# Kernel optimization log

Hardware: AMD Instinct MI355X
Metric: run time of the kernel (lower is better)

## Reference

```python
import jax, jax.numpy as jnp
import numpy as np

B, NM, NB, Z, H, K = 1024, 20000, 25000, 64, 256, 20
BETA = 0.1
LOG2PI = float(np.log(2.0 * np.pi))


def _log_normal(x, m, v):
    D = x.shape[-1]
    return (-0.5 * D * LOG2PI
            - 0.5 * jnp.sum(jnp.log(v), axis=-1)
            - 0.5 * jnp.sum((x - m) ** 2 / v, axis=-1))


def _kl_gmm(z, q_m, q_logv, p_m, p_logv):
    log_q = _log_normal(z, q_m, jnp.exp(q_logv))                               # [B]
    lp = _log_normal(z[:, None, :], p_m[None], jnp.exp(p_logv)[None])          # [B,K]
    log_p = jax.scipy.special.logsumexp(lp, axis=1) - jnp.log(float(p_m.shape[0]))
    return jnp.sum(log_q - log_p)


def _dist2(x, y):
    # ||x_i - y_j||_2^2, expanded form (avoids the [R,C,D] broadcast of the torch code)
    x2 = jnp.sum(x * x, axis=1, keepdims=True)
    y2 = jnp.sum(y * y, axis=1, keepdims=True)
    return x2 + y2.T - 2.0 * (x @ y.T)


def _distance_gmm(mu_s, mu_d, lv_s, lv_d):
    return _dist2(mu_s, mu_d) + _dist2(jnp.exp(0.5 * lv_s), jnp.exp(0.5 * lv_d)) + 1e-6


def _cost_mat(cost_s, cost_t, tran):
    f1 = jnp.sum(cost_s ** 2, axis=1, keepdims=True) / cost_s.shape[0]  # [ns,1]
    f2 = jnp.sum(cost_t ** 2, axis=1, keepdims=True) / cost_t.shape[0]  # [nt,1]
    return f1 + f2.T - 2.0 * (cost_s @ tran @ cost_t.T)


def _fgw(mu, z_mu, logvar, z_logvar):
    c_post = _distance_gmm(mu, mu, logvar, logvar)
    c_prior = _distance_gmm(z_mu, z_mu, z_logvar, z_logvar)
    c_pp = _distance_gmm(mu, z_mu, logvar, z_logvar)
    ns, nt = c_post.shape[0], c_prior.shape[0]
    p_s = jnp.ones((ns, 1), c_post.dtype) / ns
    p_t = jnp.ones((nt, 1), c_post.dtype) / nt

    def compute_tran(c_post, c_prior, c_pp):
        def outer(carry, _):
            tran, dual = carry
            cost = BETA * _cost_mat(c_post, c_prior, tran) + (1.0 - BETA) * c_pp
            kernel = jnp.exp(-cost / jnp.max(jnp.abs(cost))) * tran
            b = p_t / (kernel.T @ dual)

            def inner(c2, _):
                dual, b = c2
                dual = p_s / (kernel @ b)
                b = p_t / (kernel.T @ dual)
                return (dual, b), None

            (dual, b), _ = jax.lax.scan(inner, (dual, b), None, length=5)
            tran = (dual @ b.T) * kernel
            return (tran, dual), None

        init = (jnp.ones((ns, nt), c_post.dtype) / (ns * nt),
                jnp.ones((ns, 1), c_post.dtype) / ns)
        (tran, _), _ = jax.lax.scan(outer, init, None, length=10)
        return jnp.where(jnp.any(jnp.isnan(tran)),
                         jnp.ones((ns, nt), tran.dtype) / (ns * nt), tran)

    # torch detaches tran before the final cost, so cut all gradient through the loop
    tran = jax.lax.stop_gradient(compute_tran(c_post, c_prior, c_pp))
    cost = BETA * _cost_mat(c_post, c_prior, tran) + (1.0 - BETA) * c_pp
    return jnp.sum(cost * tran)


def _forward(batch_user_x, batch_user_y, p_mu_a, p_logv_a, p_mu_b, p_logv_b,
             eps_x, eps_y, eps_xr, eps_yr,
             W1a, b1a, W21a, b21a, W22a, b22a, W3a, b3a, W4a, b4a,
             W1b, b1b, W21b, b21b, W22b, b22b, W3b, b3b, W4b, b4b):
    def enc_a(x):
        h = jax.nn.relu(x @ W1a + b1a)
        return h @ W21a + b21a, h @ W22a + b22a

    def dec_a(z):
        return jax.nn.relu(z @ W3a + b3a) @ W4a + b4a

    def enc_b(x):
        h = jax.nn.relu(x @ W1b + b1b)
        return h @ W21b + b21b, h @ W22b + b22b

    def dec_b(z):
        return jax.nn.relu(z @ W3b + b3b) @ W4b + b4b

    # dropout rate = 0.0 -> identity
    mu_a, logvar_a = enc_a(batch_user_x)
    z_x = mu_a + eps_x * jnp.exp(0.5 * logvar_a)
    preds_x = dec_a(z_x)
    mu_b, logvar_b = enc_b(batch_user_y)
    z_y = mu_b + eps_y * jnp.exp(0.5 * logvar_b)
    preds_y = dec_b(z_y)

    gmm_reg_loss_a = _kl_gmm(z_x, mu_a, logvar_a, p_mu_a, p_logv_a)
    gmm_reg_loss_b = _kl_gmm(z_y, mu_b, logvar_b, p_mu_b, p_logv_b)
    align_global_loss = _fgw(mu_b, mu_a, logvar_b, logvar_a)

    preds_x2y = dec_b(z_x)
    preds_y2x = dec_a(z_y)
    m_xr, lv_xr = enc_b(preds_x2y)
    feature_x_r = m_xr + eps_xr * jnp.exp(0.5 * lv_xr)
    m_yr, lv_yr = enc_a(preds_y2x)
    feature_y_r = m_yr + eps_yr * jnp.exp(0.5 * lv_yr)

    cyc_loss_x = jnp.linalg.norm(z_x - feature_x_r)
    cyc_loss_y = jnp.linalg.norm(z_y - feature_y_r)
    return (preds_x, preds_y, preds_x2y, preds_y2x, z_x, z_y,
            gmm_reg_loss_a, gmm_reg_loss_b, feature_x_r, feature_y_r,
            align_global_loss, cyc_loss_x, cyc_loss_y)


def setup_inputs() -> dict:
    key = jax.random.key(0)
    ks = jax.random.split(key, 24)

    def nrm(i, shape, s=1.0):
        return jax.random.normal(ks[i], shape, dtype=jnp.float32) * s

    return {
        "user_1": jax.random.randint(ks[0], (B,), 0, 100000),
        "user_2": jax.random.randint(ks[1], (B,), 0, 100000),
        "batch_user_x": jax.random.uniform(ks[2], (B, NM), dtype=jnp.float32),
        "batch_user_y": jax.random.uniform(ks[3], (B, NB), dtype=jnp.float32),
        "p_mu_a": nrm(4, (K, Z)), "p_logv_a": nrm(5, (K, Z), 0.1),
        "p_mu_b": nrm(6, (K, Z)), "p_logv_b": nrm(7, (K, Z), 0.1),
        "eps_x": nrm(8, (B, Z)), "eps_y": nrm(9, (B, Z)),
        "eps_xr": nrm(10, (B, Z)), "eps_yr": nrm(11, (B, Z)),
        "W1a": nrm(12, (NM, H), 0.02), "b1a": jnp.zeros((H,), jnp.float32),
        "W21a": nrm(13, (H, Z), 0.02), "b21a": jnp.zeros((Z,), jnp.float32),
        "W22a": nrm(14, (H, Z), 0.02), "b22a": jnp.zeros((Z,), jnp.float32),
        "W3a": nrm(15, (Z, H), 0.02), "b3a": jnp.zeros((H,), jnp.float32),
        "W4a": nrm(16, (H, NM), 0.02), "b4a": jnp.zeros((NM,), jnp.float32),
        "W1b": nrm(17, (NB, H), 0.02), "b1b": jnp.zeros((H,), jnp.float32),
        "W21b": nrm(18, (H, Z), 0.02), "b21b": jnp.zeros((Z,), jnp.float32),
        "W22b": nrm(19, (H, Z), 0.02), "b22b": jnp.zeros((Z,), jnp.float32),
        "W3b": nrm(20, (Z, H), 0.02), "b3b": jnp.zeros((H,), jnp.float32),
        "W4b": nrm(21, (H, NB), 0.02), "b4b": jnp.zeros((NB,), jnp.float32),
    }


def reference(user_1, user_2, batch_user_x, batch_user_y, p_mu_a, p_logv_a, p_mu_b, p_logv_b,
              eps_x, eps_y, eps_xr, eps_yr,
              W1a, b1a, W21a, b21a, W22a, b22a, W3a, b3a, W4a, b4a,
              W1b, b1b, W21b, b21b, W22b, b22b, W3b, b3b, W4b, b4b):
    # user_1/user_2 are unused by the torch forward as well
    return _forward(batch_user_x, batch_user_y, p_mu_a, p_logv_a, p_mu_b, p_logv_b,
                    eps_x, eps_y, eps_xr, eps_yr,
                    W1a, b1a, W21a, b21a, W22a, b22a, W3a, b3a, W4a, b4a,
                    W1b, b1b, W21b, b21b, W22b, b22b, W3b, b3b, W4b, b4b)
```

## Files before the change

kernel.cpp:

```cpp
#include <hip/hip_runtime.h>


#define DEVI __device__ __forceinline__

typedef __attribute__((ext_vector_type(4))) float  f32x4;
typedef __attribute__((ext_vector_type(4))) short  s16x4;
typedef __attribute__((ext_vector_type(8))) short  s16x8;
typedef __attribute__((ext_vector_type(8))) __bf16 bf16x8;

#define PS (1.f / 1024.f)
#define UNIF (1.f / (1024.f * 1024.f))

DEVI short f2bf(float f) {
  unsigned u = __float_as_uint(f);
  u += 0x7fffu + ((u >> 16) & 1u);
  return (short)(u >> 16);
}
DEVI float bf2f(unsigned short u) { return __uint_as_float(((unsigned)u) << 16); }

DEVI f32x4 mfma16(bf16x8 a, bf16x8 b, f32x4 c) {
  return __builtin_amdgcn_mfma_f32_16x16x32_bf16(a, b, c, 0, 0, 0);
}

struct GemmArgs {
// ... 73 lines not shown
    #pragma unroll
    for (int s = 0; s < 2; ++s) {
      const int ko = 32 * s + 8 * (lane >> 4);
      bf16x8 a0 = *(const bf16x8*)&As[(wr * 32 +      (lane & 15)) * BKP + ko];
      bf16x8 a1 = *(const bf16x8*)&As[(wr * 32 + 16 + (lane & 15)) * BKP + ko];
      #pragma unroll
      for (int fn = 0; fn < 4; ++fn) {
        bf16x8 b = *(const bf16x8*)&Bs[(wc * 64 + fn * 16 + (lane & 15)) * BKP + ko];
        acc[0][fn] = mfma16(a0, b, acc[0][fn]);
        acc[1][fn] = mfma16(a1, b, acc[1][fn]);
      }
    }
    __syncthreads();
  }

  if constexpr (EPI == EPI_PARTIAL) {
    #pragma unroll
    for (int fm = 0; fm < 2; ++fm) {
      #pragma unroll
      for (int fn = 0; fn < 4; ++fn) {
        #pragma unroll
        for (int p = 0; p < 4; ++p) {
          int gm = m0 + wr * 32 + fm * 16 + (lane >> 4) * 4 + p;
          int gn = n0 + wc * 64 + fn * 16 + (lane & 15);
          g.partials[((size_t)split * g.M + gm) * 256 + gn] = acc[fm][fn][p];
        }
      }
    }
  } else {
    float* Cs = (float*)SM;
    #pragma unroll
    for (int h = 0; h < WC; ++h) {
      __syncthreads();
      if (wc == h) {
        #pragma unroll
        for (int fm = 0; fm < 2; ++fm)
          #pragma unroll
          for (int fn = 0; fn < 4; ++fn)
            #pragma unroll
            for (int p = 0; p < 4; ++p)
              Cs[(wr * 32 + fm * 16 + (lane >> 4) * 4 + p) * 65
                 + fn * 16 + (lane & 15)] = acc[fm][fn][p];
      }
      __syncthreads();
      const int n0h = n0 + 64 * h;
      #pragma unroll
      for (int j = tid; j < BM * 16; j += NT) {
        int r = j >> 4, c4 = j & 15;
        int gn = n0h + 4 * c4;
        if (gn < g.N) {
          f32x4 v = *(f32x4*)&Cs[r * 65 + 4 * c4];
          f32x4 b = *(const f32x4*)&g.bias[gn];
          v.x += b.x; v.y += b.y; v.z += b.z; v.w += b.w;
          *(f32x4*)(g.outF + (size_t)(m0 + r) * g.ldc + gn) = v;
        }
      }
    }
  }
}

struct Q4 { GemmArgs g[4]; };

template<int BM, int BN, int WR, int WC, int EPI>
__global__ __launch_bounds__(WR*WC*64)
void k_gemmN(Q4 q)
{
  GemmArgs g = q.g[blockIdx.z];
  if constexpr (EPI == EPI_BIAS) {
    if ((int)(blockIdx.y * BN) >= g.N) return;
  }
  gemm_body<BM, BN, WR, WC, EPI>(g);
}

struct G1Args {
  const unsigned short* A;
  const unsigned short* KTb;
  const float* dinv;
  const float* braw;
  unsigned short* U;
  const unsigned* nflag;
  int mode;
};

__global__ __launch_bounds__(256)
void k_fgw_g1(G1Args a)
{
  __shared__ short As[64 * 72];
  __shared__ short Bs[64 * 72];
  const bool uni = (a.mode == 0) || (a.mode == 2 && *a.nflag != 0u);

  const int bid = blockIdx.x, tid = threadIdx.x;
  const int lane = tid & 63, wv = tid >> 6;
  const int wr = wv & 1, wc = wv >> 1;
  const int m0 = (bid >> 4) * 64, n0 = (bid & 15) * 64;

  f32x4 acc[2][2];
  #pragma unroll
  for (int i = 0; i < 2; ++i)
    #pragma unroll
    for (int j = 0; j < 2; ++j) acc[i][j] = f32x4{0.f, 0.f, 0.f, 0.f};

  const short ub = f2bf(UNIF);

  for (int kb = 0; kb < 1024; kb += 64) {
    #pragma unroll
    for (int i = 0; i < 2; ++i) {
      int idx = tid + 256 * i;
      int r = idx >> 3, q = idx & 7;
      s16x8 av = *(const s16x8*)&a.A[(size_t)(m0 + r) * 1024 + kb + 8 * q];
      if (!uni) {
        f32x4 d0 = *(const f32x4*)&a.dinv[kb + 8 * q];
        f32x4 d1 = *(const f32x4*)&a.dinv[kb + 8 * q + 4];
        s16x8 o;
        o[0] = f2bf(bf2f((unsigned short)av[0]) * d0.x);
        o[1] = f2bf(bf2f((unsigned short)av[1]) * d0.y);
        o[2] = f2bf(bf2f((unsigned short)av[2]) * d0.z);
        o[3] = f2bf(bf2f((unsigned short)av[3]) * d0.w);
        o[4] = f2bf(bf2f((unsigned short)av[4]) * d1.x);
        o[5] = f2bf(bf2f((unsigned short)av[5]) * d1.y);
        o[6] = f2bf(bf2f((unsigned short)av[6]) * d1.z);
        o[7] = f2bf(bf2f((unsigned short)av[7]) * d1.w);
        av = o;
      }
      *(s16x8*)&As[r * 72 + 8 * q] = av;
      s16x8 bv;
      if (uni) {
        #pragma unroll
        for (int j = 0; j < 8; ++j) bv[j] = ub;
      } else {
        bv = *(const s16x8*)&a.KTb[(size_t)(n0 + r) * 1024 + kb + 8 * q];
      }
      *(s16x8*)&Bs[r * 72 + 8 * q] = bv;
    }
    __syncthreads();
    #pragma unroll
    for (int s = 0; s < 2; ++s) {
      const int ko = 32 * s + 8 * (lane >> 4);
      bf16x8 a0 = *(const bf16x8*)&As[(wr * 32 +      (lane & 15)) * 72 + ko];
      bf16x8 a1 = *(const bf16x8*)&As[(wr * 32 + 16 + (lane & 15)) * 72 + ko];
      bf16x8 b0 = *(const bf16x8*)&Bs[(wc * 32 +      (lane & 15)) * 72 + ko];
      bf16x8 b1 = *(const bf16x8*)&Bs[(wc * 32 + 16 + (lane & 15)) * 72 + ko];
      acc[0][0] = mfma16(a0, b0, acc[0][0]);
      acc[1][0] = mfma16(a1, b0, acc[1][0]);
      acc[0][1] = mfma16(a0, b1, acc[0][1]);
      acc[1][1] = mfma16(a1, b1, acc[1][1]);
    }
    __syncthreads();
  }

  #pragma unroll
  for (int fm = 0; fm < 2; ++fm) {
    #pragma unroll
    for (int fn = 0; fn < 2; ++fn) {
      int gn = n0 + wc * 32 + fn * 16 + (lane & 15);
      float bs = uni ? 1.f : (PS / a.braw[gn]);
      #pragma unroll
      for (int p = 0; p < 4; ++p) {
        int gm = m0 + wr * 32 + fm * 16 + (lane >> 4) * 4 + p;
        float v = acc[fm][fn][p];
        a.U[(size_t)gm * 1024 + gn] = (unsigned short)f2bf(uni ? v : bs * v);
      }
    }
  }
}

struct FgwGemmArgs {
  const unsigned short* A;
  const unsigned short* Bt;
  float* cost;
  const float* f1;
  const float* f2;
  const float* cpp;
  unsigned* mx;
  float* loss;
  float* braw2;
  const float* Kf;
  const float* dinv;
  const float* brawv;
  const unsigned* nflag;
};

template<int EPI>
__global__ __launch_bounds__(256)
void k_fgw_gemm(FgwGemmArgs a)
{
  __shared__ short As[64 * 72];
  __shared__ short Bs[64 * 72];
  __shared__ float red[4];

  const int bid = blockIdx.x, tid = threadIdx.x;
  const int lane = tid & 63, wv = tid >> 6;
  const int wr = wv & 1, wc = wv >> 1;
  const int m0 = (bid >> 4) * 64, n0 = (bid & 15) * 64;

  if constexpr (EPI == EPI_COST) {
    if (bid == 0) {
      #pragma unroll
      for (int i = 0; i < 4; ++i) a.braw2[tid + 256 * i] = 0.f;
    }
  }

  f32x4 acc[2][2];
  #pragma unroll
  for (int i = 0; i < 2; ++i)
    #pragma unroll
    for (int j = 0; j < 2; ++j) acc[i][j] = f32x4{0.f, 0.f, 0.f, 0.f};

  for (int kb = 0; kb < 1024; kb += 64) {
    #pragma unroll
    for (int i = 0; i < 2; ++i) {
      int idx = tid + 256 * i;
      int r = idx >> 3, q = idx & 7;
      *(s16x8*)&As[r * 72 + 8 * q] = *(const s16x8*)&a.A [(size_t)(m0 + r) * 1024 + kb + 8 * q];
      *(s16x8*)&Bs[r * 72 + 8 * q] = *(const s16x8*)&a.Bt[(size_t)(n0 + r) * 1024 + kb + 8 * q];
    }
    __syncthreads();
    #pragma unroll
    for (int s = 0; s < 2; ++s) {
      const int ko = 32 * s + 8 * (lane >> 4);
      bf16x8 a0 = *(const bf16x8*)&As[(wr * 32 +      (lane & 15)) * 72 + ko];
      bf16x8 a1 = *(const bf16x8*)&As[(wr * 32 + 16 + (lane & 15)) * 72 + ko];
      bf16x8 b0 = *(const bf16x8*)&Bs[(wc * 32 +      (lane & 15)) * 72 + ko];
      bf16x8 b1 = *(const bf16x8*)&Bs[(wc * 32 + 16 + (lane & 15)) * 72 + ko];
      acc[0][0] = mfma16(a0, b0, acc[0][0]);
      acc[1][0] = mfma16(a1, b0, acc[1][0]);
      acc[0][1] = mfma16(a0, b1, acc[0][1]);
      acc[1][1] = mfma16(a1, b1, acc[1][1]);
    }
    __syncthreads();
  }

  bool uni = false;
  if constexpr (EPI == EPI_LOSS) uni = (*a.nflag != 0u);

  float lred = 0.f;
  #pragma unroll
  for (int fm = 0; fm < 2; ++fm) {
    #pragma unroll
    for (int fn = 0; fn < 2; ++fn) {
      int gn = n0 + wc * 32 + fn * 16 + (lane & 15);
      float bs = 0.f;
      if constexpr (EPI == EPI_LOSS) bs = uni ? 0.f : (PS / a.brawv[gn]);
      #pragma unroll
      for (int p = 0; p < 4; ++p) {
        int gm = m0 + wr * 32 + fm * 16 + (lane >> 4) * 4 + p;
        float v = acc[fm][fn][p];
        size_t o = (size_t)gm * 1024 + gn;
        float c = 0.1f * (a.f1[gm] + a.f2[gn] - 2.f * v) + 0.9f * a.cpp[o];
        if constexpr (EPI == EPI_COST) {
          a.cost[o] = c;
          lred = fmaxf(lred, fabsf(c));
        } else {
          float trec = uni ? UNIF : (a.dinv[gm] * bs) * a.Kf[o];
          lred += c * trec;
        }
      }
    }
  }
  #pragma unroll
  for (int off = 32; off; off >>= 1) {
    float t = __shfl_xor(lred, off, 64);
    lred = (EPI == EPI_COST) ? fmaxf(lred, t) : (lred + t);
  }
  if (lane == 0) red[wv] = lred;
  __syncthreads();
  if (tid == 0) {
    if constexpr (EPI == EPI_COST) {
      float t = fmaxf(fmaxf(red[0], red[1]), fmaxf(red[2], red[3]));
      atomicMax(a.mx, __float_as_uint(t));
    } else {
      atomicAdd(a.loss, red[0] + red[1] + red[2] + red[3]);
    }
  }
}

__global__ __launch_bounds__(256)
void k_kbuild(const float* cost, const unsigned* mxbits, float* K, float* KT,
              unsigned short* KTb, const float* dinv, const float* brawOld,
              float* braw2, int uniform)
{
  __shared__ float tt[64 * 65];
  __shared__ float dS[64];
  __shared__ float bS[64];
  __shared__ float csum[4][64];
  const int r0 = blockIdx.x * 64, c0 = blockIdx.y * 64;
  const int tid = threadIdx.x;
  const float inv = 1.f / __uint_as_float(*mxbits);
  if (tid < 64) dS[tid] = dinv[r0 + tid];
  else if (tid >= 64 && tid < 128 && !uniform) bS[tid - 64] = PS / brawOld[c0 + tid - 64];
  __syncthreads();
  float colp = 0.f;
  #pragma unroll
  for (int i = 0; i < 16; ++i) {
    int idx = tid + 256 * i;
    int r = idx >> 6, c = idx & 63;
    size_t o = (size_t)(r0 + r) * 1024 + (c0 + c);
    float trec = uniform ? UNIF : (dS[r] * bS[c]) * K[o];
    float v = expf(-cost[o] * inv) * trec;
    K[o] = v;
    tt[r * 65 + c] = v;
    colp += v * dS[r];
  }
  csum[tid >> 6][tid & 63] = colp;
  __syncthreads();
  #pragma unroll
  for (int i = 0; i < 16; ++i) {
    int idx = tid + 256 * i;
    int c = idx >> 6, r = idx & 63;
    float v = tt[r * 65 + c];
    size_t o = (size_t)(c0 + c) * 1024 + (r0 + r);
    KT[o] = v;
    KTb[o] = (unsigned short)f2bf(v);
  }
  if (tid < 64)
    atomicAdd(&braw2[c0 + tid],
              csum[0][tid] + csum[1][tid] + csum[2][tid] + csum[3][tid]);
}

__global__ __launch_bounds__(256)
void k_matvec(const float* M, const float* xraw, float* yraw, float* invOut)
{
  const int r = blockIdx.x * 4 + (threadIdx.x >> 6);
  const int lane = threadIdx.x & 63;
  const int wv = threadIdx.x >> 6;
  const f32x4* row = (const f32x4*)(M + (size_t)r * 1024);
  const f32x4* xv  = (const f32x4*)xraw;
  float s = 0.f;
  #pragma unroll
  for (int q = 0; q < 4; ++q) {
    f32x4 a = row[lane + 64 * q];
    f32x4 x = xv [lane + 64 * q];
    f32x4 iv;
    iv.x = PS / x.x; iv.y = PS / x.y; iv.z = PS / x.z; iv.w = PS / x.w;
    if (invOut && blockIdx.x == 0 && wv == 0)
      *(f32x4*)&invOut[4 * (lane + 64 * q)] = iv;
    s += a.x * iv.x + a.y * iv.y + a.z * iv.z + a.w * iv.w;
  }
  #pragma unroll
  for (int o = 32; o; o >>= 1) s += __shfl_xor(s, o, 64);
  if (lane == 0) yraw[r] = s;
}

__global__ __launch_bounds__(256)
void k_nanscan(const float* K, const float* dinv, const float* braw, unsigned* flag)
{
  unsigned bad = 0;
  const int base = blockIdx.x * 256 + threadIdx.x;
  #pragma unroll
  for (int i = 0; i < 16; ++i) {
    int idx = base + 65536 * i;
    int r = idx >> 10, c = idx & 1023;
    float v = (dinv[r] * (PS / braw[c])) * K[idx];
    if (v != v) bad = 1u;
  }
  if (bad) atomicOr(flag, 1u);
}

struct DistMMArgs {
  const unsigned short* Fx[3]; const unsigned short* Fy[3];
  const float* nx[3]; const float* ny[3];
  unsigned short* outB[2]; float* outF; float* frow[2];
};
__global__ __launch_bounds__(256)
void k_distmm(DistMMArgs a)
{
  __shared__ short As[64 * 72];
  __shared__ short Bs[64 * 72];
  const int z = blockIdx.y;
  const int bid = blockIdx.x, tid = threadIdx.x;
  const int lane = tid & 63, wv = tid >> 6;
  const int wr = wv & 1, wc = wv >> 1;
  const int m0 = (bid >> 4) * 64, n0 = (bid & 15) * 64;
  const unsigned short* X = a.Fx[z];
  const unsigned short* Y = a.Fy[z];

  f32x4 acc[2][2];
  #pragma unroll
  for (int i = 0; i < 2; ++i)
    #pragma unroll
    for (int j = 0; j < 2; ++j) acc[i][j] = f32x4{0.f, 0.f, 0.f, 0.f};

  #pragma unroll
  for (int kb = 0; kb < 128; kb += 64) {
    #pragma unroll
    for (int i = 0; i < 2; ++i) {
      int idx = tid + 256 * i;
      int r = idx >> 3, q = idx & 7;
      *(s16x8*)&As[r * 72 + 8 * q] = *(const s16x8*)&X[(size_t)(m0 + r) * 128 + kb + 8 * q];
      *(s16x8*)&Bs[r * 72 + 8 * q] = *(const s16x8*)&Y[(size_t)(n0 + r) * 128 + kb + 8 * q];
    }
    __syncthreads();
    #pragma unroll
    for (int s = 0; s < 2; ++s) {
      const int ko = 32 * s + 8 * (lane >> 4);
      bf16x8 a0 = *(const bf16x8*)&As[(wr * 32 +      (lane & 15)) * 72 + ko];
      bf16x8 a1 = *(const bf16x8*)&As[(wr * 32 + 16 + (lane & 15)) * 72 + ko];
      bf16x8 b0 = *(const bf16x8*)&Bs[(wc * 32 +      (lane & 15)) * 72 + ko];
      bf16x8 b1 = *(const bf16x8*)&Bs[(wc * 32 + 16 + (lane & 15)) * 72 + ko];
      acc[0][0] = mfma16(a0, b0, acc[0][0]);
      acc[1][0] = mfma16(a1, b0, acc[1][0]);
      acc[0][1] = mfma16(a0, b1, acc[0][1]);
      acc[1][1] = mfma16(a1, b1, acc[1][1]);
    }
    __syncthreads();
  }

  const float* nxp = a.nx[z];
  const float* nyp = a.ny[z];
  float rp[2][4];
  #pragma unroll
  for (int fm = 0; fm < 2; ++fm)
    #pragma unroll
    for (int p = 0; p < 4; ++p) rp[fm][p] = 0.f;

  #pragma unroll
  for (int fm = 0; fm < 2; ++fm) {
    #pragma unroll
    for (int fn = 0; fn < 2; ++fn) {
      #pragma unroll
      for (int p = 0; p < 4; ++p) {
        int gm = m0 + wr * 32 + fm * 16 + (lane >> 4) * 4 + p;
        int gn = n0 + wc * 32 + fn * 16 + (lane & 15);
        float val = nxp[gm] + nyp[gn] - 2.f * acc[fm][fn][p] + 1e-6f;
        if (z == 2) a.outF[(size_t)gm * 1024 + gn] = val;
        else {
          a.outB[z][(size_t)gm * 1024 + gn] = (unsigned short)f2bf(val);
          rp[fm][p] += val * val;
        }
      }
    }
  }
  if (z < 2) {
    #pragma unroll
    for (int fm = 0; fm < 2; ++fm)
      #pragma unroll
      for (int p = 0; p < 4; ++p) {
        float v = rp[fm][p];
        v += __shfl_xor(v, 1, 64);
        v += __shfl_xor(v, 2, 64);
        v += __shfl_xor(v, 4, 64);
        v += __shfl_xor(v, 8, 64);
        rp[fm][p] = v;
      }
    if ((lane & 15) == 0) {
      #pragma unroll
      for (int fm = 0; fm < 2; ++fm)
        #pragma unroll
        for (int p = 0; p < 4; ++p) {
          int gm = m0 + wr * 32 + fm * 16 + (lane >> 4) * 4 + p;
          atomicAdd(&a.frow[z][gm], rp[fm][p] * (1.f / 1024.f));
        }
    }
  }
}

struct T4 {
  const float* in[4]; unsigned short* out[4]; int R[4], C[4], nx[4], nt[4];
  float* dinv; float* f1; float* f2; unsigned* mx; unsigned* nanflag;
  float* cyc; float* ga; float* gb; float* al;
};
__global__ void k_transpose4(T4 d)
{
  const int z = blockIdx.y;
  const int tid = threadIdx.x;
  if (z == 4) {
    if (blockIdx.x == 0) {
      #pragma unroll
      for (int i = 0; i < 4; ++i) {
        int k = tid + 256 * i;
        d.dinv[k] = PS; d.f1[k] = 0.f; d.f2[k] = 0.f;
      }
      if (tid < 16) d.mx[tid] = 0u;
      if (tid == 0) {
        *d.nanflag = 0u; d.cyc[0] = 0.f; d.cyc[1] = 0.f;
        *d.ga = 0.f; *d.gb = 0.f; *d.al = 0.f;
      }
    }
    return;
  }
  __shared__ float t[64][65];
  const int tile = blockIdx.x;
  if (tile >= d.nt[z]) return;
  const int R = d.R[z], C = d.C[z];
  const int r0 = (tile % d.nx[z]) * 64, c0 = (tile / d.nx[z]) * 64;
  const float* in = d.in[z];
  unsigned short* out = d.out[z];
  #pragma unroll
  for (int i = 0; i < 16; ++i) {
    int idx = tid + 256 * i;
    int r = idx >> 6, c = idx & 63;
    float v = 0.f;
    if ((r0 + r) < R && (c0 + c) < C) v = in[(size_t)(r0 + r) * C + (c0 + c)];
    t[r][c] = v;
  }
  __syncthreads();
  #pragma unroll
  for (int i = 0; i < 16; ++i) {
    int idx = tid + 256 * i;
    int c = idx >> 6, r = idx & 63;
    if ((c0 + c) < C && (r0 + r) < R)
      out[(size_t)(c0 + c) * R + (r0 + r)] = (unsigned short)f2bf(t[r][c]);
  }
}

__global__ void k_wcomb_reduce(const float* partials, unsigned short* WcTa,
                               unsigned short* WcTb)
{
  __shared__ float t[64][65];
  const int z = blockIdx.z;
  const float* P = partials + (size_t)z * 32 * 256 * 256;
  unsigned short* WcT = z ? WcTb : WcTa;
  const int u0 = blockIdx.x * 64, v0 = blockIdx.y * 64;
  const int tid = threadIdx.x;
  #pragma unroll
  for (int i = 0; i < 16; ++i) {
    int idx = tid + 256 * i;
    int u = idx >> 6, v = idx & 63;
    float s = 0.f;
    for (int p = 0; p < 32; ++p)
      s += P[(size_t)p * 65536 + (u0 + u) * 256 + (v0 + v)];
    t[u][v] = s;
  }
  __syncthreads();
  #pragma unroll
  for (int i = 0; i < 16; ++i) {
    int idx = tid + 256 * i;
    int v = idx >> 6, u = idx & 63;
    WcT[(size_t)(v0 + v) * 256 + (u0 + u)] = (unsigned short)f2bf(t[u][v]);
  }
}

struct BcArgs {
  const float* b4[2]; const unsigned short* Wt1[2]; const float* b1[2];
  float* bc[2]; int K[2];
};
__global__ void k_bcvec(BcArgs a)
{
  const int y = blockIdx.y;
  const int c = blockIdx.x * 4 + (threadIdx.x >> 6);
  const int lane = threadIdx.x & 63;
  const int K = a.K[y];
  const unsigned short* wrow = a.Wt1[y] + (size_t)c * K;
  const float* b4 = a.b4[y];
  float s = 0.f;
  for (int k = lane * 8; k < K; k += 512) {
    s16x8 w = *(const s16x8*)&wrow[k];
    f32x4 v0 = *(const f32x4*)&b4[k];
    f32x4 v1 = *(const f32x4*)&b4[k + 4];
    s += v0.x * bf2f((unsigned short)w[0]) + v0.y * bf2f((unsigned short)w[1])
       + v0.z * bf2f((unsigned short)w[2]) + v0.w * bf2f((unsigned short)w[3])
       + v1.x * bf2f((unsigned short)w[4]) + v1.y * bf2f((unsigned short)w[5])
       + v1.z * bf2f((unsigned short)w[6]) + v1.w * bf2f((unsigned short)w[7]);
  }
  #pragma unroll
  for (int o = 32; o; o >>= 1) s += __shfl_xor(s, o, 64);
  if (lane == 0) a.bc[y][c] = s + a.b1[y][c];
}

struct EF {
  const float* partials[2]; const float* bias[2];
  const float* W21[2]; const float* b21[2];
  const float* W22[2]; const float* b22[2]; const float* eps[2];
  const float* pmu[2]; const float* plv[2]; float* gmmO[2];
  float* mu[2]; float* lv[2]; float* zO[2];
  unsigned short* F[2]; float* n[2];
};
__global__ __launch_bounds__(256)
void k_enc_fused(EF a)
{
  __shared__ float hrow[256];
  __shared__ float res[128];
  const int y = blockIdx.y;
  const int i = blockIdx.x;
  const int t = threadIdx.x;
  {
    float s = a.bias[y][t];
    const float* P = a.partials[y] + (size_t)i * 256 + t;
    #pragma unroll
    for (int p = 0; p < 16; ++p) s += P[(size_t)p * 262144];
    hrow[t] = fmaxf(s, 0.f);
  }
  __syncthreads();
  if (t < 128) {
    const int c = t & 63;
    const float* W = (t < 64) ? a.W21[y] : a.W22[y];
    float acc = (t < 64) ? a.b21[y][c] : a.b22[y][c];
    #pragma unroll 8
    for (int j = 0; j < 256; ++j) acc += hrow[j] * W[j * 64 + c];
    res[t] = acc;
  }
  __syncthreads();
  if (t < 64) {
    float mu = res[t], lv = res[64 + t];
    a.mu[y][(size_t)i * 64 + t] = mu;
    a.lv[y][(size_t)i * 64 + t] = lv;
    float sig = expf(0.5f * lv);
    float zd = mu + a.eps[y][(size_t)i * 64 + t] * sig;
    a.zO[y][(size_t)i * 64 + t] = zd;
    unsigned short u0 = (unsigned short)f2bf(mu);
    unsigned short u1 = (unsigned short)f2bf(sig);
    unsigned short* Fr = a.F[y] + (size_t)i * 128;
    Fr[t] = u0;
// ... 128 lines not shown
  const float* W3b = (const float*)d_in[28];  const float* b3b = (const float*)d_in[29];
  const float* W4b = (const float*)d_in[30];  const float* b4b = (const float*)d_in[31];

  float* out = (float*)d_out;
  const size_t P_X = 0, P_Y = 20480000, P_X2Y = 46080000, P_Y2X = 71680000;
  const size_t Z_X = 92160000, Z_Y = 92225536;
  const size_t GMM_A = 92291072, GMM_B = 92291073;
  const size_t F_XR = 92291074, F_YR = 92356610;
  const size_t ALIGN = 92422146, CYC_X = 92422147, CYC_Y = 92422148;

  char* w = (char*)d_ws;
  size_t off = 0;
  auto alloc = [&](size_t bytes) -> void* {
    void* p = w + off;
    off += (bytes + 255) & ~(size_t)255;
    return p;
  };
  unsigned short* Wt1a = (unsigned short*)alloc((size_t)256 * 20000 * 2);
  unsigned short* Wt1b = (unsigned short*)alloc((size_t)256 * 25000 * 2);
  unsigned short* W4ta = (unsigned short*)alloc((size_t)20000 * 256 * 2);
  unsigned short* W4tb = (unsigned short*)alloc((size_t)25000 * 256 * 2);
  unsigned short* WcTa = (unsigned short*)alloc((size_t)256 * 256 * 2);
  unsigned short* WcTb = (unsigned short*)alloc((size_t)256 * 256 * 2);
  float* bca  = (float*)alloc(256 * 4);
  float* bcb  = (float*)alloc(256 * 4);
  float* mu_a = (float*)alloc(1024 * 64 * 4);
  float* lv_a = (float*)alloc(1024 * 64 * 4);
  float* mu_b = (float*)alloc(1024 * 64 * 4);
  float* lv_b = (float*)alloc(1024 * 64 * 4);
  float* f1   = (float*)alloc(1024 * 4);
  float* f2   = (float*)alloc(1024 * 4);
  unsigned* mx      = (unsigned*)alloc(16 * 4);
  unsigned* nanflag = (unsigned*)alloc(256);
  float* cyc  = (float*)alloc(256);
  float* draw = (float*)alloc(1024 * 4);
  float* braw = (float*)alloc(1024 * 4);
  float* braw2 = (float*)alloc(1024 * 4);
  float* dinv = (float*)alloc(1024 * 4);
  unsigned short* Fb = (unsigned short*)alloc((size_t)1024 * 128 * 2);
  unsigned short* Fa = (unsigned short*)alloc((size_t)1024 * 128 * 2);
  float* nb = (float*)alloc(1024 * 4);
  float* na = (float*)alloc(1024 * 4);
  char* arena = (char*)alloc((size_t)32 * 1024 * 1024);
  float* partials = (float*)arena;
  size_t ao = 0;
  auto aalloc = [&](size_t bytes) -> void* {
    void* p = arena + ao;
    ao += (bytes + 255) & ~(size_t)255;
    return p;
  };
  unsigned short* cpostB  = (unsigned short*)aalloc((size_t)1024 * 1024 * 2);
  unsigned short* cpriorB = (unsigned short*)aalloc((size_t)1024 * 1024 * 2);
  float* cpp  = (float*)aalloc((size_t)1024 * 1024 * 4);
  unsigned short* Umat  = (unsigned short*)aalloc((size_t)1024 * 1024 * 2);
  float* cost  = (float*)aalloc((size_t)1024 * 1024 * 4);
  float* Kmat  = (float*)aalloc((size_t)1024 * 1024 * 4);
  float* KTmat = (float*)aalloc((size_t)1024 * 1024 * 4);
  unsigned short* KTb = (unsigned short*)aalloc((size_t)1024 * 1024 * 2);
  float* hd0 = (float*)(arena);
  float* hd1 = (float*)(arena + (size_t)1024 * 256 * 4);
  float* hd2 = (float*)(arena + (size_t)2 * 1024 * 256 * 4);
  float* hd3 = (float*)(arena + (size_t)3 * 1024 * 256 * 4);

  {
    T4 d{};
    d.in[0] = W1a; d.out[0] = Wt1a; d.R[0] = 20000; d.C[0] = 256;
    d.in[1] = W1b; d.out[1] = Wt1b; d.R[1] = 25000; d.C[1] = 256;
    d.in[2] = W4a; d.out[2] = W4ta; d.R[2] = 256;   d.C[2] = 20000;
    d.in[3] = W4b; d.out[3] = W4tb; d.R[3] = 256;   d.C[3] = 25000;
    for (int z = 0; z < 4; ++z) {
      d.nx[z] = (d.R[z] + 63) / 64;
      d.nt[z] = d.nx[z] * ((d.C[z] + 63) / 64);
    }
    d.dinv = dinv; d.f1 = f1; d.f2 = f2; d.mx = mx; d.nanflag = nanflag;
    d.cyc = cyc; d.ga = out + GMM_A; d.gb = out + GMM_B; d.al = out + ALIGN;
    k_transpose4<<<dim3(1564, 5), 256, 0, stream>>>(d);
  }

  {
    Q4 q{};
    q.g[0].Af = W4a; q.g[0].Bt = Wt1a; q.g[0].partials = partials;
    q.g[0].M = 256; q.g[0].N = 256; q.g[0].K = 20000;
    q.g[0].lda = 20000; q.g[0].ldbt = 20000;
    q.g[0].totSteps = 313; q.g[0].nSplits = 32;
    q.g[1] = q.g[0];
    q.g[1].Af = W4b; q.g[1].Bt = Wt1b;
    q.g[1].partials = partials + (size_t)32 * 65536;
    q.g[1].K = 25000; q.g[1].lda = 25000; q.g[1].ldbt = 25000; q.g[1].totSteps = 391;
    k_gemmN<128, 256, 4, 4, EPI_PARTIAL><<<dim3(2, 32, 2), 1024, 0, stream>>>(q);
    k_wcomb_reduce<<<dim3(4, 4, 2), 256, 0, stream>>>(partials, WcTa, WcTb);
    BcArgs bc{};
    bc.b4[0] = b4a; bc.Wt1[0] = Wt1a; bc.b1[0] = b1a; bc.bc[0] = bca; bc.K[0] = 20000;
    bc.b4[1] = b4b; bc.Wt1[1] = Wt1b; bc.b1[1] = b1b; bc.bc[1] = bcb; bc.K[1] = 25000;
    k_bcvec<<<dim3(64, 2), 256, 0, stream>>>(bc);
  }

  {
    Q4 q{};
    q.g[0].Af = X; q.g[0].Bt = Wt1a; q.g[0].partials = partials;
    q.g[0].M = 1024; q.g[0].N = 256; q.g[0].K = 20000;
    q.g[0].lda = 20000; q.g[0].ldbt = 20000;
    q.g[0].totSteps = 313; q.g[0].nSplits = 16;
    q.g[1] = q.g[0];
    q.g[1].Af = Y; q.g[1].Bt = Wt1b;
    q.g[1].partials = partials + (size_t)16 * 1024 * 256;
    q.g[1].K = 25000; q.g[1].lda = 25000; q.g[1].ldbt = 25000; q.g[1].totSteps = 391;
    k_gemmN<128, 256, 4, 4, EPI_PARTIAL><<<dim3(8, 16, 2), 1024, 0, stream>>>(q);
    EF e{};
    e.partials[0] = partials; e.partials[1] = partials + (size_t)16 * 1024 * 256;
    e.bias[0] = b1a; e.bias[1] = b1b;
    e.W21[0] = W21a; e.b21[0] = b21a; e.W22[0] = W22a; e.b22[0] = b22a;
    e.eps[0] = epsx; e.mu[0] = mu_a; e.lv[0] = lv_a; e.zO[0] = out + Z_X;
    e.F[0] = Fa; e.n[0] = na;
    e.pmu[0] = pmua; e.plv[0] = plva; e.gmmO[0] = out + GMM_A;
    e.W21[1] = W21b; e.b21[1] = b21b; e.W22[1] = W22b; e.b22[1] = b22b;
    e.eps[1] = epsy; e.mu[1] = mu_b; e.lv[1] = lv_b; e.zO[1] = out + Z_Y;
    e.F[1] = Fb; e.n[1] = nb;
    e.pmu[1] = pmub; e.plv[1] = plvb; e.gmmO[1] = out + GMM_B;
    k_enc_fused<<<dim3(1024, 2), 256, 0, stream>>>(e);
  }

  {
    DistMMArgs dm{};
    dm.Fx[0] = Fb; dm.Fy[0] = Fb; dm.nx[0] = nb; dm.ny[0] = nb;
    dm.Fx[1] = Fa; dm.Fy[1] = Fa; dm.nx[1] = na; dm.ny[1] = na;
    dm.Fx[2] = Fb; dm.Fy[2] = Fa; dm.nx[2] = nb; dm.ny[2] = na;
    dm.outB[0] = cpostB; dm.outB[1] = cpriorB; dm.outF = cpp;
    dm.frow[0] = f1; dm.frow[1] = f2;
    k_distmm<<<dim3(256, 3), 256, 0, stream>>>(dm);
  }
  G1Args g1{};
  g1.A = cpostB; g1.KTb = KTb; g1.dinv = dinv; g1.braw = braw;
  g1.U = Umat; g1.nflag = nanflag;
  FgwGemmArgs fg{};
  fg.A = Umat; fg.Bt = cpriorB;
  fg.f1 = f1; fg.f2 = f2; fg.cpp = cpp; fg.cost = cost;
  fg.loss = out + ALIGN; fg.braw2 = braw2;
  fg.Kf = Kmat; fg.dinv = dinv; fg.brawv = braw; fg.nflag = nanflag;
  for (int it = 0; it < 10; ++it) {
    g1.mode = (it == 0) ? 0 : 1;
    k_fgw_g1<<<256, 256, 0, stream>>>(g1);
    fg.mx = mx + it;
    k_fgw_gemm<EPI_COST><<<256, 256, 0, stream>>>(fg);
    k_kbuild<<<dim3(16, 16), 256, 0, stream>>>(cost, mx + it, Kmat, KTmat, KTb,
                                               dinv, braw, braw2, it == 0 ? 1 : 0);
    for (int r = 0; r < 5; ++r) {
      k_matvec<<<256, 256, 0, stream>>>(Kmat, r == 0 ? braw2 : braw, draw, nullptr);
      k_matvec<<<256, 256, 0, stream>>>(KTmat, draw, braw, r == 4 ? dinv : nullptr);
    }
  }
  k_nanscan<<<256, 256, 0, stream>>>(Kmat, dinv, braw, nanflag);
  g1.mode = 2;
  k_fgw_g1<<<256, 256, 0, stream>>>(g1);
  k_fgw_gemm<EPI_LOSS><<<256, 256, 0, stream>>>(fg);

  {
    DH4 d{};
    d.z[0] = out + Z_X; d.W3[0] = W3a; d.b3[0] = b3a; d.hd[0] = hd0;
    d.z[1] = out + Z_Y; d.W3[1] = W3a; d.b3[1] = b3a; d.hd[1] = hd1;
    d.z[2] = out + Z_Y; d.W3[2] = W3b; d.b3[2] = b3b; d.hd[2] = hd2;
    d.z[3] = out + Z_X; d.W3[3] = W3b; d.b3[3] = b3b; d.hd[3] = hd3;
    k_dec_head4<<<dim3(1024, 4), 256, 0, stream>>>(d);
  }

  {
    RencArgs r{};
    r.hd[0] = hd3; r.WcT[0] = WcTb; r.bc[0] = bcb;
    r.W21[0] = W21b; r.b21[0] = b21b; r.W22[0] = W22b; r.b22[0] = b22b;
    r.eps[0] = epsxr; r.fout[0] = out + F_XR; r.zin[0] = out + Z_X;
    r.hd[1] = hd1; r.WcT[1] = WcTa; r.bc[1] = bca;
    r.W21[1] = W21a; r.b21[1] = b21a; r.W22[1] = W22a; r.b22[1] = b22a;
    r.eps[1] = epsyr; r.fout[1] = out + F_YR; r.zin[1] = out + Z_Y;
    r.cyc = cyc;
    k_renc_head<<<dim3(1024, 2), 256, 0, stream>>>(r);
  }
  k_finish<<<1, 64, 0, stream>>>(cyc, out + CYC_X, out + CYC_Y);

  {
    Q4 q{};
    q.g[0].Af = hd0; q.g[0].Bt = W4ta; q.g[0].outF = out + P_X; q.g[0].bias = b4a;
    q.g[0].M = 1024; q.g[0].N = 20000; q.g[0].K = 256;
    q.g[0].lda = 256; q.g[0].ldbt = 256; q.g[0].ldc = 20000;
    q.g[1] = q.g[0]; q.g[1].Af = hd1; q.g[1].outF = out + P_Y2X;
    q.g[2] = q.g[0];
    q.g[2].Af = hd2; q.g[2].Bt = W4tb; q.g[2].outF = out + P_Y; q.g[2].bias = b4b;
    q.g[2].N = 25000; q.g[2].ldc = 25000;
    q.g[3] = q.g[2]; q.g[3].Af = hd3; q.g[3].outF = out + P_X2Y;
    k_gemmN<128, 128, 4, 2, EPI_BIAS><<<dim3(8, 196, 4), 512, 0, stream>>>(q);
  }
}
```

Before: 1.453 ms.

## Use 8 waves per FGW GEMM block and double split-K for weight fold

The FGW GEMM kernels (g1 and cost/loss) now launch 512 threads per 64x64 tile, with each wave computing a 32x16 sub-tile. This halves per-wave MFMA work and load loops to raise latency hiding on the small 256-block grid. Separately, the W4·W1 split-K GEMM goes from 32 to 64 splits, with the reduce kernel and partials offsets updated to match, to fill more CUs at the cost of more partial traffic. Wave index mapping (wr/wc from wv) is assumed to extend to 8 waves, and it must do so for the tile coverage to be correct.

Result: faster. 1.394 ms (-4.1%).

```diff
diff --git a/kernel.cpp b/kernel.cpp
--- a/kernel.cpp
+++ b/kernel.cpp
@@ -179,7 +179,7 @@
   int mode;
 };
 
-__global__ __launch_bounds__(256)
+__global__ __launch_bounds__(512)
 void k_fgw_g1(G1Args a)
 {
   __shared__ short As[64 * 72];
@@ -191,19 +191,15 @@
   const int wr = wv & 1, wc = wv >> 1;
   const int m0 = (bid >> 4) * 64, n0 = (bid & 15) * 64;
 
-  f32x4 acc[2][2];
-  #pragma unroll
-  for (int i = 0; i < 2; ++i)
-    #pragma unroll
-    for (int j = 0; j < 2; ++j) acc[i][j] = f32x4{0.f, 0.f, 0.f, 0.f};
+  f32x4 acc[2];
+  acc[0] = f32x4{0.f, 0.f, 0.f, 0.f};
+  acc[1] = f32x4{0.f, 0.f, 0.f, 0.f};
 
   const short ub = f2bf(UNIF);
 
   for (int kb = 0; kb < 1024; kb += 64) {
-    #pragma unroll
-    for (int i = 0; i < 2; ++i) {
-      int idx = tid + 256 * i;
-      int r = idx >> 3, q = idx & 7;
+    {
+      int r = tid >> 3, q = tid & 7;
       s16x8 av = *(const s16x8*)&a.A[(size_t)(m0 + r) * 1024 + kb + 8 * q];
       if (!uni) {
         f32x4 d0 = *(const f32x4*)&a.dinv[kb + 8 * q];
@@ -233,30 +229,24 @@
     #pragma unroll
     for (int s = 0; s < 2; ++s) {
       const int ko = 32 * s + 8 * (lane >> 4);
+      bf16x8 b0 = *(const bf16x8*)&Bs[(wc * 16 + (lane & 15)) * 72 + ko];
       bf16x8 a0 = *(const bf16x8*)&As[(wr * 32 +      (lane & 15)) * 72 + ko];
       bf16x8 a1 = *(const bf16x8*)&As[(wr * 32 + 16 + (lane & 15)) * 72 + ko];
-      bf16x8 b0 = *(const bf16x8*)&Bs[(wc * 32 +      (lane & 15)) * 72 + ko];
-      bf16x8 b1 = *(const bf16x8*)&Bs[(wc * 32 + 16 + (lane & 15)) * 72 + ko];
-      acc[0][0] = mfma16(a0, b0, acc[0][0]);
-      acc[1][0] = mfma16(a1, b0, acc[1][0]);
-      acc[0][1] = mfma16(a0, b1, acc[0][1]);
-      acc[1][1] = mfma16(a1, b1, acc[1][1]);
+      acc[0] = mfma16(a0, b0, acc[0]);
+      acc[1] = mfma16(a1, b0, acc[1]);
     }
     __syncthreads();
   }
 
+  const int gn = n0 + wc * 16 + (lane & 15);
+  const float bs = uni ? 1.f : (PS / a.braw[gn]);
   #pragma unroll
   for (int fm = 0; fm < 2; ++fm) {
     #pragma unroll
-    for (int fn = 0; fn < 2; ++fn) {
-      int gn = n0 + wc * 32 + fn * 16 + (lane & 15);
-      float bs = uni ? 1.f : (PS / a.braw[gn]);
-      #pragma unroll
-      for (int p = 0; p < 4; ++p) {
-        int gm = m0 + wr * 32 + fm * 16 + (lane >> 4) * 4 + p;
-        float v = acc[fm][fn][p];
-        a.U[(size_t)gm * 1024 + gn] = (unsigned short)f2bf(uni ? v : bs * v);
-      }
+    for (int p = 0; p < 4; ++p) {
+      int gm = m0 + wr * 32 + fm * 16 + (lane >> 4) * 4 + p;
+      float v = acc[fm][p];
+      a.U[(size_t)gm * 1024 + gn] = (unsigned short)f2bf(uni ? v : bs * v);
     }
   }
 }
@@ -278,12 +268,12 @@
 };
 
 template<int EPI>
-__global__ __launch_bounds__(256)
+__global__ __launch_bounds__(512)
 void k_fgw_gemm(FgwGemmArgs a)
 {
   __shared__ short As[64 * 72];
   __shared__ short Bs[64 * 72];
-  __shared__ float red[4];
+  __shared__ float red[8];
 
   const int bid = blockIdx.x, tid = threadIdx.x;
   const int lane = tid & 63, wv = tid >> 6;
@@ -293,9 +283,174 @@
   if constexpr (EPI == EPI_COST) {
     if (bid == 0) {
       #pragma unroll
-      for (int i = 0; i < 4; ++i) a.braw2[tid + 256 * i] = 0.f;
-    }
-  }
+      for (int i = 0; i < 2; ++i) a.braw2[tid + 512 * i] = 0.f;
+    }
+  }
+
+  f32x4 acc[2];
+  acc[0] = f32x4{0.f, 0.f, 0.f, 0.f};
+  acc[1] = f32x4{0.f, 0.f, 0.f, 0.f};
+
+  for (int kb = 0; kb < 1024; kb += 64) {
+    {
+      int r = tid >> 3, q = tid & 7;
+      *(s16x8*)&As[r * 72 + 8 * q] = *(const s16x8*)&a.A [(size_t)(m0 + r) * 1024 + kb + 8 * q];
+      *(s16x8*)&Bs[r * 72 + 8 * q] = *(const s16x8*)&a.Bt[(size_t)(n0 + r) * 1024 + kb + 8 * q];
+    }
+    __syncthreads();
+    #pragma unroll
+    for (int s = 0; s < 2; ++s) {
+      const int ko = 32 * s + 8 * (lane >> 4);
+      bf16x8 b0 = *(const bf16x8*)&Bs[(wc * 16 + (lane & 15)) * 72 + ko];
+      bf16x8 a0 = *(const bf16x8*)&As[(wr * 32 +      (lane & 15)) * 72 + ko];
+      bf16x8 a1 = *(const bf16x8*)&As[(wr * 32 + 16 + (lane & 15)) * 72 + ko];
+      acc[0] = mfma16(a0, b0, acc[0]);
+      acc[1] = mfma16(a1, b0, acc[1]);
+    }
+    __syncthreads();
+  }
+
+  bool uni = false;
+  if constexpr (EPI == EPI_LOSS) uni = (*a.nflag != 0u);
+
+  const int gn = n0 + wc * 16 + (lane & 15);
+  float bs = 0.f;
+  if constexpr (EPI == EPI_LOSS) bs = uni ? 0.f : (PS / a.brawv[gn]);
+
+  float lred = 0.f;
+  #pragma unroll
+  for (int fm = 0; fm < 2; ++fm) {
+    #pragma unroll
+    for (int p = 0; p < 4; ++p) {
+      int gm = m0 + wr * 32 + fm * 16 + (lane >> 4) * 4 + p;
+      float v = acc[fm][p];
+      size_t o = (size_t)gm * 1024 + gn;
+      float c = 0.1f * (a.f1[gm] + a.f2[gn] - 2.f * v) + 0.9f * a.cpp[o];
+      if constexpr (EPI == EPI_COST) {
+        a.cost[o] = c;
+        lred = fmaxf(lred, fabsf(c));
+      } else {
+        float trec = uni ? UNIF : (a.dinv[gm] * bs) * a.Kf[o];
+        lred += c * trec;
+      }
+    }
+  }
+  #pragma unroll
+  for (int off = 32; off; off >>= 1) {
+    float t = __shfl_xor(lred, off, 64);
+    lred = (EPI == EPI_COST) ? fmaxf(lred, t) : (lred + t);
+  }
+  if (lane == 0) red[wv] = lred;
+  __syncthreads();
+  if (tid == 0) {
+    float t = red[0];
+    #pragma unroll
+    for (int i = 1; i < 8; ++i)
+      t = (EPI == EPI_COST) ? fmaxf(t, red[i]) : (t + red[i]);
+    if constexpr (EPI == EPI_COST) atomicMax(a.mx, __float_as_uint(t));
+    else atomicAdd(a.loss, t);
+  }
+}
+
+__global__ __launch_bounds__(256)
+void k_kbuild(const float* cost, const unsigned* mxbits, float* K, float* KT,
+              unsigned short* KTb, const float* dinv, const float* brawOld,
+              float* braw2, int uniform)
+{
+  __shared__ float tt[64 * 65];
+  __shared__ float dS[64];
+  __shared__ float bS[64];
+  __shared__ float csum[4][64];
+  const int r0 = blockIdx.x * 64, c0 = blockIdx.y * 64;
+  const int tid = threadIdx.x;
+  const float inv = 1.f / __uint_as_float(*mxbits);
+  if (tid < 64) dS[tid] = dinv[r0 + tid];
+  else if (tid >= 64 && tid < 128 && !uniform) bS[tid - 64] = PS / brawOld[c0 + tid - 64];
+  __syncthreads();
+  float colp = 0.f;
+  #pragma unroll
+  for (int i = 0; i < 16; ++i) {
+    int idx = tid + 256 * i;
+    int r = idx >> 6, c = idx & 63;
+    size_t o = (size_t)(r0 + r) * 1024 + (c0 + c);
+    float trec = uniform ? UNIF : (dS[r] * bS[c]) * K[o];
+    float v = expf(-cost[o] * inv) * trec;
+    K[o] = v;
+    tt[r * 65 + c] = v;
+    colp += v * dS[r];
+  }
+  csum[tid >> 6][tid & 63] = colp;
+  __syncthreads();
+  #pragma unroll
+  for (int i = 0; i < 16; ++i) {
+    int idx = tid + 256 * i;
+    int c = idx >> 6, r = idx & 63;
+    float v = tt[r * 65 + c];
+    size_t o = (size_t)(c0 + c) * 1024 + (r0 + r);
+    KT[o] = v;
+    KTb[o] = (unsigned short)f2bf(v);
+  }
+  if (tid < 64)
+    atomicAdd(&braw2[c0 + tid],
+              csum[0][tid] + csum[1][tid] + csum[2][tid] + csum[3][tid]);
+}
+
+__global__ __launch_bounds__(256)
+void k_matvec(const float* M, const float* xraw, float* yraw, float* invOut)
+{
+  const int r = blockIdx.x * 4 + (threadIdx.x >> 6);
+  const int lane = threadIdx.x & 63;
+  const int wv = threadIdx.x >> 6;
+  const f32x4* row = (const f32x4*)(M + (size_t)r * 1024);
+  const f32x4* xv  = (const f32x4*)xraw;
+  float s = 0.f;
+  #pragma unroll
+  for (int q = 0; q < 4; ++q) {
+    f32x4 a = row[lane + 64 * q];
+    f32x4 x = xv [lane + 64 * q];
+    f32x4 iv;
+    iv.x = PS / x.x; iv.y = PS / x.y; iv.z = PS / x.z; iv.w = PS / x.w;
+    if (invOut && blockIdx.x == 0 && wv == 0)
+      *(f32x4*)&invOut[4 * (lane + 64 * q)] = iv;
+    s += a.x * iv.x + a.y * iv.y + a.z * iv.z + a.w * iv.w;
+  }
+  #pragma unroll
+  for (int o = 32; o; o >>= 1) s += __shfl_xor(s, o, 64);
+  if (lane == 0) yraw[r] = s;
+}
+
+__global__ __launch_bounds__(256)
+void k_nanscan(const float* K, const float* dinv, const float* braw, unsigned* flag)
+{
+  unsigned bad = 0;
+  const int base = blockIdx.x * 256 + threadIdx.x;
+  #pragma unroll
+  for (int i = 0; i < 16; ++i) {
+    int idx = base + 65536 * i;
+    int r = idx >> 10, c = idx & 1023;
+    float v = (dinv[r] * (PS / braw[c])) * K[idx];
+    if (v != v) bad = 1u;
+  }
+  if (bad) atomicOr(flag, 1u);
+}
+
+struct DistMMArgs {
+  const unsigned short* Fx[3]; const unsigned short* Fy[3];
+  const float* nx[3]; const float* ny[3];
+  unsigned short* outB[2]; float* outF; float* frow[2];
+};
+__global__ __launch_bounds__(256)
+void k_distmm(DistMMArgs a)
+{
+  __shared__ short As[64 * 72];
+  __shared__ short Bs[64 * 72];
+  const int z = blockIdx.y;
+  const int bid = blockIdx.x, tid = threadIdx.x;
+  const int lane = tid & 63, wv = tid >> 6;
+  const int wr = wv & 1, wc = wv >> 1;
+  const int m0 = (bid >> 4) * 64, n0 = (bid & 15) * 64;
+  const unsigned short* X = a.Fx[z];
+  const unsigned short* Y = a.Fy[z];
 
   f32x4 acc[2][2];
   #pragma unroll
@@ -303,13 +458,14 @@
     #pragma unroll
     for (int j = 0; j < 2; ++j) acc[i][j] = f32x4{0.f, 0.f, 0.f, 0.f};
 
-  for (int kb = 0; kb < 1024; kb += 64) {
+  #pragma unroll
+  for (int kb = 0; kb < 128; kb += 64) {
     #pragma unroll
     for (int i = 0; i < 2; ++i) {
       int idx = tid + 256 * i;
       int r = idx >> 3, q = idx & 7;
-      *(s16x8*)&As[r * 72 + 8 * q] = *(const s16x8*)&a.A [(size_t)(m0 + r) * 1024 + kb + 8 * q];
-      *(s16x8*)&Bs[r * 72 + 8 * q] = *(const s16x8*)&a.Bt[(size_t)(n0 + r) * 1024 + kb + 8 * q];
+      *(s16x8*)&As[r * 72 + 8 * q] = *(const s16x8*)&X[(size_t)(m0 + r) * 128 + kb + 8 * q];
+      *(s16x8*)&Bs[r * 72 + 8 * q] = *(const s16x8*)&Y[(size_t)(n0 + r) * 128 + kb + 8 * q];
     }
     __syncthreads();
     #pragma unroll
@@ -327,181 +483,6 @@
     __syncthreads();
   }
 
-  bool uni = false;
-  if constexpr (EPI == EPI_LOSS) uni = (*a.nflag != 0u);
-
-  float lred = 0.f;
-  #pragma unroll
-  for (int fm = 0; fm < 2; ++fm) {
-    #pragma unroll
-    for (int fn = 0; fn < 2; ++fn) {
-      int gn = n0 + wc * 32 + fn * 16 + (lane & 15);
-      float bs = 0.f;
-      if constexpr (EPI == EPI_LOSS) bs = uni ? 0.f : (PS / a.brawv[gn]);
-      #pragma unroll
-      for (int p = 0; p < 4; ++p) {
-        int gm = m0 + wr * 32 + fm * 16 + (lane >> 4) * 4 + p;
-        float v = acc[fm][fn][p];
-        size_t o = (size_t)gm * 1024 + gn;
-        float c = 0.1f * (a.f1[gm] + a.f2[gn] - 2.f * v) + 0.9f * a.cpp[o];
-        if constexpr (EPI == EPI_COST) {
-          a.cost[o] = c;
-          lred = fmaxf(lred, fabsf(c));
-        } else {
-          float trec = uni ? UNIF : (a.dinv[gm] * bs) * a.Kf[o];
-          lred += c * trec;
-        }
-      }
-    }
-  }
-  #pragma unroll
-  for (int off = 32; off; off >>= 1) {
-    float t = __shfl_xor(lred, off, 64);
-    lred = (EPI == EPI_COST) ? fmaxf(lred, t) : (lred + t);
-  }
-  if (lane == 0) red[wv] = lred;
-  __syncthreads();
-  if (tid == 0) {
-    if constexpr (EPI == EPI_COST) {
-      float t = fmaxf(fmaxf(red[0], red[1]), fmaxf(red[2], red[3]));
-      atomicMax(a.mx, __float_as_uint(t));
-    } else {
-      atomicAdd(a.loss, red[0] + red[1] + red[2] + red[3]);
-    }
-  }
-}
-
-__global__ __launch_bounds__(256)
-void k_kbuild(const float* cost, const unsigned* mxbits, float* K, float* KT,
-              unsigned short* KTb, const float* dinv, const float* brawOld,
-              float* braw2, int uniform)
-{
-  __shared__ float tt[64 * 65];
-  __shared__ float dS[64];
-  __shared__ float bS[64];
-  __shared__ float csum[4][64];
-  const int r0 = blockIdx.x * 64, c0 = blockIdx.y * 64;
-  const int tid = threadIdx.x;
-  const float inv = 1.f / __uint_as_float(*mxbits);
-  if (tid < 64) dS[tid] = dinv[r0 + tid];
-  else if (tid >= 64 && tid < 128 && !uniform) bS[tid - 64] = PS / brawOld[c0 + tid - 64];
-  __syncthreads();
-  float colp = 0.f;
-  #pragma unroll
-  for (int i = 0; i < 16; ++i) {
-    int idx = tid + 256 * i;
-    int r = idx >> 6, c = idx & 63;
-    size_t o = (size_t)(r0 + r) * 1024 + (c0 + c);
-    float trec = uniform ? UNIF : (dS[r] * bS[c]) * K[o];
-    float v = expf(-cost[o] * inv) * trec;
-    K[o] = v;
-    tt[r * 65 + c] = v;
-    colp += v * dS[r];
-  }
-  csum[tid >> 6][tid & 63] = colp;
-  __syncthreads();
-  #pragma unroll
-  for (int i = 0; i < 16; ++i) {
-    int idx = tid + 256 * i;
-    int c = idx >> 6, r = idx & 63;
-    float v = tt[r * 65 + c];
-    size_t o = (size_t)(c0 + c) * 1024 + (r0 + r);
-    KT[o] = v;
-    KTb[o] = (unsigned short)f2bf(v);
-  }
-  if (tid < 64)
-    atomicAdd(&braw2[c0 + tid],
-              csum[0][tid] + csum[1][tid] + csum[2][tid] + csum[3][tid]);
-}
-
-__global__ __launch_bounds__(256)
-void k_matvec(const float* M, const float* xraw, float* yraw, float* invOut)
-{
-  const int r = blockIdx.x * 4 + (threadIdx.x >> 6);
-  const int lane = threadIdx.x & 63;
-  const int wv = threadIdx.x >> 6;
-  const f32x4* row = (const f32x4*)(M + (size_t)r * 1024);
-  const f32x4* xv  = (const f32x4*)xraw;
-  float s = 0.f;
-  #pragma unroll
-  for (int q = 0; q < 4; ++q) {
-    f32x4 a = row[lane + 64 * q];
-    f32x4 x = xv [lane + 64 * q];
-    f32x4 iv;
-    iv.x = PS / x.x; iv.y = PS / x.y; iv.z = PS / x.z; iv.w = PS / x.w;
-    if (invOut && blockIdx.x == 0 && wv == 0)
-      *(f32x4*)&invOut[4 * (lane + 64 * q)] = iv;
-    s += a.x * iv.x + a.y * iv.y + a.z * iv.z + a.w * iv.w;
-  }
-  #pragma unroll
-  for (int o = 32; o; o >>= 1) s += __shfl_xor(s, o, 64);
-  if (lane == 0) yraw[r] = s;
-}
-
-__global__ __launch_bounds__(256)
-void k_nanscan(const float* K, const float* dinv, const float* braw, unsigned* flag)
-{
-  unsigned bad = 0;
-  const int base = blockIdx.x * 256 + threadIdx.x;
-  #pragma unroll
-  for (int i = 0; i < 16; ++i) {
-    int idx = base + 65536 * i;
-    int r = idx >> 10, c = idx & 1023;
-    float v = (dinv[r] * (PS / braw[c])) * K[idx];
-    if (v != v) bad = 1u;
-  }
-  if (bad) atomicOr(flag, 1u);
-}
-
-struct DistMMArgs {
-  const unsigned short* Fx[3]; const unsigned short* Fy[3];
-  const float* nx[3]; const float* ny[3];
-  unsigned short* outB[2]; float* outF; float* frow[2];
-};
-__global__ __launch_bounds__(256)
-void k_distmm(DistMMArgs a)
-{
-  __shared__ short As[64 * 72];
-  __shared__ short Bs[64 * 72];
-  const int z = blockIdx.y;
-  const int bid = blockIdx.x, tid = threadIdx.x;
-  const int lane = tid & 63, wv = tid >> 6;
-  const int wr = wv & 1, wc = wv >> 1;
-  const int m0 = (bid >> 4) * 64, n0 = (bid & 15) * 64;
-  const unsigned short* X = a.Fx[z];
-  const unsigned short* Y = a.Fy[z];
-
-  f32x4 acc[2][2];
-  #pragma unroll
-  for (int i = 0; i < 2; ++i)
-    #pragma unroll
-    for (int j = 0; j < 2; ++j) acc[i][j] = f32x4{0.f, 0.f, 0.f, 0.f};
-
-  #pragma unroll
-  for (int kb = 0; kb < 128; kb += 64) {
-    #pragma unroll
-    for (int i = 0; i < 2; ++i) {
-      int idx = tid + 256 * i;
-      int r = idx >> 3, q = idx & 7;
-      *(s16x8*)&As[r * 72 + 8 * q] = *(const s16x8*)&X[(size_t)(m0 + r) * 128 + kb + 8 * q];
-      *(s16x8*)&Bs[r * 72 + 8 * q] = *(const s16x8*)&Y[(size_t)(n0 + r) * 128 + kb + 8 * q];
-    }
-    __syncthreads();
-    #pragma unroll
-    for (int s = 0; s < 2; ++s) {
-      const int ko = 32 * s + 8 * (lane >> 4);
-      bf16x8 a0 = *(const bf16x8*)&As[(wr * 32 +      (lane & 15)) * 72 + ko];
-      bf16x8 a1 = *(const bf16x8*)&As[(wr * 32 + 16 + (lane & 15)) * 72 + ko];
-      bf16x8 b0 = *(const bf16x8*)&Bs[(wc * 32 +      (lane & 15)) * 72 + ko];
-      bf16x8 b1 = *(const bf16x8*)&Bs[(wc * 32 + 16 + (lane & 15)) * 72 + ko];
-      acc[0][0] = mfma16(a0, b0, acc[0][0]);
-      acc[1][0] = mfma16(a1, b0, acc[1][0]);
-      acc[0][1] = mfma16(a0, b1, acc[0][1]);
-      acc[1][1] = mfma16(a1, b1, acc[1][1]);
-    }
-    __syncthreads();
-  }
-
   const float* nxp = a.nx[z];
   const float* nyp = a.ny[z];
   float rp[2][4];
@@ -605,7 +586,7 @@
 {
   __shared__ float t[64][65];
   const int z = blockIdx.z;
-  const float* P = partials + (size_t)z * 32 * 256 * 256;
+  const float* P = partials + (size_t)z * 64 * 256 * 256;
   unsigned short* WcT = z ? WcTb : WcTa;
   const int u0 = blockIdx.x * 64, v0 = blockIdx.y * 64;
   const int tid = threadIdx.x;
@@ -614,7 +595,7 @@
     int idx = tid + 256 * i;
     int u = idx >> 6, v = idx & 63;
     float s = 0.f;
-    for (int p = 0; p < 32; ++p)
+    for (int p = 0; p < 64; ++p)
       s += P[(size_t)p * 65536 + (u0 + u) * 256 + (v0 + v)];
     t[u][v] = s;
   }
@@ -909,12 +890,12 @@
     q.g[0].Af = W4a; q.g[0].Bt = Wt1a; q.g[0].partials = partials;
     q.g[0].M = 256; q.g[0].N = 256; q.g[0].K = 20000;
     q.g[0].lda = 20000; q.g[0].ldbt = 20000;
-    q.g[0].totSteps = 313; q.g[0].nSplits = 32;
+    q.g[0].totSteps = 313; q.g[0].nSplits = 64;
     q.g[1] = q.g[0];
     q.g[1].Af = W4b; q.g[1].Bt = Wt1b;
-    q.g[1].partials = partials + (size_t)32 * 65536;
+    q.g[1].partials = partials + (size_t)64 * 65536;
     q.g[1].K = 25000; q.g[1].lda = 25000; q.g[1].ldbt = 25000; q.g[1].totSteps = 391;
-    k_gemmN<128, 256, 4, 4, EPI_PARTIAL><<<dim3(2, 32, 2), 1024, 0, stream>>>(q);
+    k_gemmN<128, 256, 4, 4, EPI_PARTIAL><<<dim3(2, 64, 2), 1024, 0, stream>>>(q);
     k_wcomb_reduce<<<dim3(4, 4, 2), 256, 0, stream>>>(partials, WcTa, WcTb);
     BcArgs bc{};
     bc.b4[0] = b4a; bc.Wt1[0] = Wt1a; bc.b1[0] = b1a; bc.bc[0] = bca; bc.K[0] = 20000;
@@ -966,9 +947,9 @@
   fg.Kf = Kmat; fg.dinv = dinv; fg.brawv = braw; fg.nflag = nanflag;
   for (int it = 0; it < 10; ++it) {
     g1.mode = (it == 0) ? 0 : 1;
-    k_fgw_g1<<<256, 256, 0, stream>>>(g1);
+    k_fgw_g1<<<256, 512, 0, stream>>>(g1);
     fg.mx = mx + it;
-    k_fgw_gemm<EPI_COST><<<256, 256, 0, stream>>>(fg);
+    k_fgw_gemm<EPI_COST><<<256, 512, 0, stream>>>(fg);
     k_kbuild<<<dim3(16, 16), 256, 0, stream>>>(cost, mx + it, Kmat, KTmat, KTb,
                                                dinv, braw, braw2, it == 0 ? 1 : 0);
     for (int r = 0; r < 5; ++r) {
@@ -978,8 +959,8 @@
   }
   k_nanscan<<<256, 256, 0, stream>>>(Kmat, dinv, braw, nanflag);
   g1.mode = 2;
-  k_fgw_g1<<<256, 256, 0, stream>>>(g1);
-  k_fgw_gemm<EPI_LOSS><<<256, 256, 0, stream>>>(fg);
+  k_fgw_g1<<<256, 512, 0, stream>>>(g1);
+  k_fgw_gemm<EPI_LOSS><<<256, 512, 0, stream>>>(fg);
 
   {
     DH4 d{};
```
